# Kernel optimization log

Measured on AMD Instinct MI355X. Metric: run time of the kernel, lower is better.

Reference implementation:

```python
import jax, jax.numpy as jnp
import numpy as np

D_MODEL = 1024
LN_EPS = 1e-5


def setup_inputs() -> dict:
    key = jax.random.key(0)
    k_u, k_b, k_c = jax.random.split(key, 3)
    B, L, D = 8, 4096, D_MODEL
    u = jax.random.normal(k_u, (B, L, D), dtype=jnp.float32)
    # parameters (torch init analogues)
    log_a = jnp.log(jnp.linspace(0.9, 0.99, D, dtype=jnp.float32))
    bound = 1.0 / np.sqrt(D)
    W_b = jax.random.uniform(k_b, (D, D), minval=-bound, maxval=bound, dtype=jnp.float32)
    W_c = jax.random.uniform(k_c, (D, D), minval=-bound, maxval=bound, dtype=jnp.float32)
    gamma = jnp.ones((D,), dtype=jnp.float32)
    beta = jnp.zeros((D,), dtype=jnp.float32)
    return {"u": u, "log_a": log_a, "W_b": W_b, "W_c": W_c, "gamma": gamma, "beta": beta}


def reference(u, log_a, W_b, W_c, gamma, beta):
    # u: [B, L, D]; diagonal LTI SSM: state_t = a * state_{t-1} + (u_t @ W_b^T)
    B, L, D = u.shape
    a = jnp.exp(log_a)  # [D]
    u_b = jnp.einsum('bld,ed->ble', u, W_b)  # batched b-projection over all timesteps

    def step(state, ub_t):
        state = a * state + ub_t
        return state, state

    init = jnp.zeros((B, D), dtype=u.dtype)
    _, states = jax.lax.scan(step, init, jnp.swapaxes(u_b, 0, 1))  # [L, B, D]
    states = jnp.swapaxes(states, 0, 1)  # [B, L, D]

    y = jnp.einsum('bld,ed->ble', states, W_c)  # c-projection batched over time

    # LayerNorm over last dim
    mean = jnp.mean(y, axis=-1, keepdims=True)
    var = jnp.mean(jnp.square(y - mean), axis=-1, keepdims=True)
    return gamma * (y - mean) * jax.lax.rsqrt(var + LN_EPS) + beta
```

## Files before the change

kernel.cpp:

```cpp
#include <hip/hip_runtime.h>
#include <hip/hip_bf16.h>
#include <math.h>

#define B_SZ 8
#define L_SZ 4096
#define D_SZ 1024
#define CHT  64
#define NCH  (L_SZ / CHT)

typedef __bf16 bf16_t;
typedef bf16_t bf16x8 __attribute__((ext_vector_type(8)));
typedef bf16_t bf16x4 __attribute__((ext_vector_type(4)));
typedef float  f32x4  __attribute__((ext_vector_type(4)));

#define BM 256
#define BN 256
#define BK 32
#define NT (1024 / BK)
#define BUFB 32768
#define EP_P 68

__device__ __forceinline__ void gld16(const void* g, void* l) {
  __builtin_amdgcn_global_load_lds(
      (const __attribute__((address_space(1))) void*)g,
      (__attribute__((address_space(3))) void*)l, 16, 0, 0);
}

template<int MODE>
__global__ __launch_bounds__(512, 2)
void gemm256(const bf16_t* __restrict__ A, const bf16_t* __restrict__ Wt,
             bf16_t* __restrict__ Cg, const float* __restrict__ pw,
             float* __restrict__ cf) {
  __shared__ __align__(16) char smem[98304];
  const int tid  = threadIdx.x;
  const int lane = tid & 63;
  const int wave = tid >> 6;
  const int wm = wave >> 2, wn = wave & 3;
  const int fr = lane & 15, g = lane >> 4;

  const int flat = (blockIdx.x & 7) * 64 + (blockIdx.x >> 3);
  const int bx = flat & 3, by = flat >> 2;
  const int brow = by * BM, bcol = bx * BN;

  const int rA = lane >> 2, cA = lane & 3;
  const int sS = (rA ^ (lane >> 4)) & 3;
  const int scol = ((cA ^ sS) << 3);
  const bf16_t* a0 = A  + (size_t)(brow + wave * 16 + rA) * 1024 + scol;
  const bf16_t* a1 = a0 + (size_t)128 * 1024;
  const bf16_t* b0 = Wt + (size_t)(bcol + wave * 16 + rA) * 1024 + scol;
  const bf16_t* b1 = b0 + (size_t)128 * 1024;

  const int sR  = (fr ^ (fr >> 2)) & 3;
  const int rch = ((g ^ sR) << 4);
  const int aoffB = (wm * 128 + fr) * 64 + rch;
  const int boffB = (wn * 64 + fr) * 64 + rch;

  f32x4 acc[8][4] = {};

#define STAGE(BU, T) { \
    char* d_ = smem + (BU) * BUFB + wave * 1024; \
    const int ko_ = (T) * BK; \
    gld16(a0 + ko_, d_); \
    gld16(a1 + ko_, d_ + 8192); \
    gld16(b0 + ko_, d_ + 16384); \
    gld16(b1 + ko_, d_ + 24576); \
  }

  STAGE(0, 0)
  STAGE(1, 1)
  asm volatile("s_waitcnt vmcnt(4)" ::: "memory");
  __builtin_amdgcn_s_barrier();
  asm volatile("" ::: "memory");

  int bu = 0, bs = 2;
  for (int t = 0; t < NT; ++t) {
    const char* aB = smem + bu * BUFB;
    const char* bB = aB + 16384;
    bf16x8 af[8], bfv[4];
#pragma unroll
    for (int mi = 0; mi < 8; ++mi) af[mi] = *(const bf16x8*)(aB + aoffB + mi * 1024);
#pragma unroll
    for (int ni = 0; ni < 4; ++ni) bfv[ni] = *(const bf16x8*)(bB + boffB + ni * 1024);
    if (t + 2 < NT) STAGE(bs, t + 2)
    __builtin_amdgcn_s_setprio(1);
#pragma unroll
    for (int mi = 0; mi < 8; ++mi)
#pragma unroll
      for (int ni = 0; ni < 4; ++ni)
        acc[mi][ni] = __builtin_amdgcn_mfma_f32_16x16x32_bf16(af[mi], bfv[ni], acc[mi][ni], 0, 0, 0);
    __builtin_amdgcn_s_setprio(0);
    if (t + 2 < NT) asm volatile("s_waitcnt vmcnt(4)" ::: "memory");
    else            asm volatile("s_waitcnt vmcnt(0)" ::: "memory");
    __builtin_amdgcn_s_barrier();
    asm volatile("" ::: "memory");
    bu = (bu == 2) ? 0 : bu + 1;
    bs = (bs == 2) ? 0 : bs + 1;
  }
#undef STAGE

  __syncthreads();
  float* strip = (float*)smem;
  const int bb  = by >> 4;
  const int cg0 = (by & 15) * 4;
#pragma unroll 1
  for (int q = 0; q < 4; ++q) {
    if (wn == q) {
#pragma unroll
      for (int mi = 0; mi < 8; ++mi)
#pragma unroll
        for (int ni = 0; ni < 4; ++ni)
#pragma unroll
          for (int r = 0; r < 4; ++r)
            strip[(wm * 128 + mi * 16 + g * 4 + r) * EP_P + ni * 16 + fr] = acc[mi][ni][r];
    }
    __syncthreads();
    if constexpr (MODE == 0) {
      if (tid < 256) {
        const int col = tid & 63;
        const int ch  = tid >> 6;
        const int d   = bcol + q * 64 + col;
        const float a = pw[d];
        float s = 0.f;
#pragma unroll 1
        for (int grp = 0; grp < 4; ++grp) {
          float v[16];
#pragma unroll
          for (int u = 0; u < 16; ++u) v[u] = strip[(ch * 64 + grp * 16 + u) * EP_P + col];
#pragma unroll
          for (int u = 0; u < 16; ++u) { s = a * s + v[u]; v[u] = s; }
#pragma unroll
          for (int u = 0; u < 16; ++u) strip[(ch * 64 + grp * 16 + u) * EP_P + col] = v[u];
        }
        cf[((size_t)(bb * NCH + cg0 + ch)) * D_SZ + d] = s;
      }
      __syncthreads();
    }
#pragma unroll
    for (int j = 0; j < 4; ++j) {
      const int u = j * 512 + tid;
      const int row = u >> 3;
      const int cu = (u & 7) * 8;
      f32x4 lo = *(const f32x4*)&strip[row * EP_P + cu];
      f32x4 hi = *(const f32x4*)&strip[row * EP_P + cu + 4];
      bf16x8 h;
#pragma unroll
      for (int jj = 0; jj < 4; ++jj) { h[jj] = (bf16_t)lo[jj]; h[4 + jj] = (bf16_t)hi[jj]; }
      *(bf16x8*)&Cg[(size_t)(brow + row) * 1024 + bcol + q * 64 + cu] = h;
    }
    __syncthreads();
  }
}

__global__ __launch_bounds__(256)
void conv_bf16_k(const float* __restrict__ src, bf16_t* __restrict__ dst, int n) {
  int i = (blockIdx.x * 256 + threadIdx.x) * 4;
  const int stride = gridDim.x * 256 * 4;
  for (; i < n; i += stride) {
    f32x4 v = *(const f32x4*)(src + i);
    bf16x4 h;
#pragma unroll
    for (int j = 0; j < 4; ++j) h[j] = (bf16_t)v[j];
    *(bf16x4*)(dst + i) = h;
  }
}

__global__ __launch_bounds__(256)
void pow_k(const float* __restrict__ log_a, float* __restrict__ pw) {
  const int t = blockIdx.x;
  const int d = threadIdx.x * 4;
#pragma unroll
  for (int j = 0; j < 4; ++j)
    pw[t * D_SZ + d + j] = expf(log_a[d + j] * (float)(t + 1));
}

__global__ __launch_bounds__(256)
void scan_carry_k(const float* __restrict__ log_a, float* __restrict__ cf) {
  const int d = blockIdx.x * 256 + threadIdx.x;
  const int b = blockIdx.y;
  const float aT = expf(log_a[d] * (float)CHT);
  float s = 0.f;
  for (int c = 0; c < NCH; ++c) {
    const size_t idx = ((size_t)(b * NCH + c)) * D_SZ + d;
    s = aT * s + cf[idx];
    cf[idx] = s;
  }
}

__global__ __launch_bounds__(256)
void scan_apply_k(const bf16_t* __restrict__ xb16, const float* __restrict__ pw,
                  const float* __restrict__ cf, bf16_t* __restrict__ xs16) {
  const int d4 = threadIdx.x * 4;
  const int l = blockIdx.x;
  const int b = blockIdx.y;
  const int c = l >> 6;
  const int t = l & (CHT - 1);
  const size_t idx = ((size_t)(b * L_SZ + l)) * D_SZ + d4;
  bf16x4 hv = *(const bf16x4*)(xb16 + idx);
  f32x4 s;
#pragma unroll
  for (int j = 0; j < 4; ++j) s[j] = (float)hv[j];
  if (c > 0) {
    f32x4 p  = *(const f32x4*)(pw + t * D_SZ + d4);
    f32x4 cv = *(const f32x4*)(cf + ((size_t)(b * NCH + (c - 1))) * D_SZ + d4);
    s += p * cv;
  }
  bf16x4 h;
#pragma unroll
  for (int j = 0; j < 4; ++j) h[j] = (bf16_t)s[j];
  *(bf16x4*)(xs16 + idx) = h;
}

__global__ __launch_bounds__(256)
void ln_k(const bf16_t* __restrict__ y, const float* __restrict__ gamma,
          const float* __restrict__ beta, float* __restrict__ out) {
  const size_t row = blockIdx.x;
  const int tid = threadIdx.x;
  bf16x4 h = *(const bf16x4*)(y + row * D_SZ + tid * 4);
  float v[4];
#pragma unroll
  for (int j = 0; j < 4; ++j) v[j] = (float)h[j];
  float s  = v[0] + v[1] + v[2] + v[3];
  float sq = v[0] * v[0] + v[1] * v[1] + v[2] * v[2] + v[3] * v[3];
#pragma unroll
  for (int off = 32; off; off >>= 1) {
    s  += __shfl_down(s, off);
    sq += __shfl_down(sq, off);
  }
  __shared__ float red[8];
  const int wid = tid >> 6;
  if ((tid & 63) == 0) { red[wid] = s; red[4 + wid] = sq; }
  __syncthreads();
  s  = red[0] + red[1] + red[2] + red[3];
  sq = red[4] + red[5] + red[6] + red[7];
  const float mean = s * (1.f / D_SZ);
  const float var  = sq * (1.f / D_SZ) - mean * mean;
  const float inv  = rsqrtf(var + 1e-5f);
  f32x4 gm = *(const f32x4*)(gamma + tid * 4);
  f32x4 bt = *(const f32x4*)(beta  + tid * 4);
  f32x4 o;
#pragma unroll
  for (int j = 0; j < 4; ++j) o[j] = (v[j] - mean) * inv * gm[j] + bt[j];
  *(f32x4*)(out + row * D_SZ + tid * 4) = o;
}

extern "C" void kernel_launch(void* const* d_in, const int* in_sizes, int n_in,
                              void* d_out, int out_size, void* d_ws, size_t ws_size,
                              hipStream_t stream) {
  const float* u     = (const float*)d_in[0];
  const float* log_a = (const float*)d_in[1];
  const float* W_b   = (const float*)d_in[2];
  const float* W_c   = (const float*)d_in[3];
  const float* gamma = (const float*)d_in[4];
  const float* beta  = (const float*)d_in[5];
  float* out = (float*)d_out;

  const size_t NBLD = (size_t)B_SZ * L_SZ * D_SZ;
  bf16_t* u16  = (bf16_t*)d_ws;
  bf16_t* xb16 = u16 + NBLD;
  bf16_t* wb16 = xb16 + NBLD;
  bf16_t* wc16 = wb16 + (size_t)D_SZ * D_SZ;
  float*  cf   = (float*)(wc16 + (size_t)D_SZ * D_SZ);
  float*  pw   = cf + (size_t)B_SZ * NCH * D_SZ;
  bf16_t* xs16 = u16;
  bf16_t* y16  = xb16;

  const int nblk = (B_SZ * L_SZ / BM) * (D_SZ / BN);

  conv_bf16_k<<<2048, 256, 0, stream>>>(u, u16, (int)NBLD);
  conv_bf16_k<<<512, 256, 0, stream>>>(W_b, wb16, D_SZ * D_SZ);
  conv_bf16_k<<<512, 256, 0, stream>>>(W_c, wc16, D_SZ * D_SZ);
  pow_k<<<CHT, 256, 0, stream>>>(log_a, pw);

  gemm256<0><<<nblk, 512, 0, stream>>>(u16, wb16, xb16, pw, cf);
  scan_carry_k<<<dim3(D_SZ / 256, B_SZ), 256, 0, stream>>>(log_a, cf);
  scan_apply_k<<<dim3(L_SZ, B_SZ), 256, 0, stream>>>(xb16, pw, cf, xs16);
  gemm256<1><<<nblk, 512, 0, stream>>>(xs16, wc16, y16, nullptr, nullptr);
  ln_k<<<B_SZ * L_SZ, 256, 0, stream>>>(y16, gamma, beta, out);
}
```

Before: 268.0 us.

## Retile GEMM to 256x128x64 with 2x4 wave grid and widen scan_apply vectors

Changes the GEMM block tile from 256x256 with K-step 32 to 256x128 with K-step 64. The wave layout becomes 4x2, each wave holds a 64x64 sub-tile, and the LDS swizzle and staging are rebuilt for 128-byte rows across three 48KB buffers. This doubles the grid and halves per-thread accumulators, aiming for better occupancy and fewer loop iterations and barriers. The cost is lower arithmetic intensity per block and more LDS per block, which may limit residency. scan_apply now processes 8 bf16 elements per thread with 128 threads for wider memory accesses.

```diff
diff --git a/kernel.cpp b/kernel.cpp
--- a/kernel.cpp
+++ b/kernel.cpp
@@ -14,10 +14,10 @@
 typedef float  f32x4  __attribute__((ext_vector_type(4)));
 
 #define BM 256
-#define BN 256
-#define BK 32
+#define BN 128
+#define BK 64
 #define NT (1024 / BK)
-#define BUFB 32768
+#define BUFB 49152
 #define EP_P 68
 
 __device__ __forceinline__ void gld16(const void* g, void* l) {
@@ -31,65 +31,72 @@
 void gemm256(const bf16_t* __restrict__ A, const bf16_t* __restrict__ Wt,
              bf16_t* __restrict__ Cg, const float* __restrict__ pw,
              float* __restrict__ cf) {
-  __shared__ __align__(16) char smem[98304];
+  __shared__ __align__(16) char smem[3 * BUFB];
   const int tid  = threadIdx.x;
   const int lane = tid & 63;
   const int wave = tid >> 6;
-  const int wm = wave >> 2, wn = wave & 3;
+  const int wm = wave >> 1, wn = wave & 1;
   const int fr = lane & 15, g = lane >> 4;
 
-  const int flat = (blockIdx.x & 7) * 64 + (blockIdx.x >> 3);
-  const int bx = flat & 3, by = flat >> 2;
+  const int flat = (blockIdx.x & 7) * 128 + (blockIdx.x >> 3);
+  const int bx = flat & 7, by = flat >> 3;
   const int brow = by * BM, bcol = bx * BN;
 
-  const int rA = lane >> 2, cA = lane & 3;
-  const int sS = (rA ^ (lane >> 4)) & 3;
-  const int scol = ((cA ^ sS) << 3);
-  const bf16_t* a0 = A  + (size_t)(brow + wave * 16 + rA) * 1024 + scol;
-  const bf16_t* a1 = a0 + (size_t)128 * 1024;
-  const bf16_t* b0 = Wt + (size_t)(bcol + wave * 16 + rA) * 1024 + scol;
-  const bf16_t* b1 = b0 + (size_t)128 * 1024;
-
-  const int sR  = (fr ^ (fr >> 2)) & 3;
-  const int rch = ((g ^ sR) << 4);
-  const int aoffB = (wm * 128 + fr) * 64 + rch;
-  const int boffB = (wn * 64 + fr) * 64 + rch;
-
-  f32x4 acc[8][4] = {};
+  const int sr = lane >> 3;
+  const int sc = (lane & 7) ^ sr;
+  const bf16_t* a0 = A  + (size_t)(brow + wave * 8 + sr) * 1024 + sc * 8;
+  const bf16_t* b0 = Wt + (size_t)(bcol + wave * 8 + sr) * 1024 + sc * 8;
+
+  const int c0 = ((g)     ^ (fr & 7)) << 4;
+  const int c1 = ((4 + g) ^ (fr & 7)) << 4;
+  const int arowB = (wm * 64 + fr) * 128;
+  const int browB = (wn * 64 + fr) * 128;
+
+  f32x4 acc[4][4] = {};
 
 #define STAGE(BU, T) { \
     char* d_ = smem + (BU) * BUFB + wave * 1024; \
-    const int ko_ = (T) * BK; \
+    const size_t ko_ = (size_t)(T) * BK; \
     gld16(a0 + ko_, d_); \
-    gld16(a1 + ko_, d_ + 8192); \
-    gld16(b0 + ko_, d_ + 16384); \
-    gld16(b1 + ko_, d_ + 24576); \
+    gld16(a0 + (size_t)64 * 1024 + ko_, d_ + 8192); \
+    gld16(a0 + (size_t)128 * 1024 + ko_, d_ + 16384); \
+    gld16(a0 + (size_t)192 * 1024 + ko_, d_ + 24576); \
+    gld16(b0 + ko_, d_ + 32768); \
+    gld16(b0 + (size_t)64 * 1024 + ko_, d_ + 40960); \
   }
 
   STAGE(0, 0)
   STAGE(1, 1)
-  asm volatile("s_waitcnt vmcnt(4)" ::: "memory");
+  asm volatile("s_waitcnt vmcnt(6)" ::: "memory");
   __builtin_amdgcn_s_barrier();
   asm volatile("" ::: "memory");
 
   int bu = 0, bs = 2;
   for (int t = 0; t < NT; ++t) {
     const char* aB = smem + bu * BUFB;
-    const char* bB = aB + 16384;
-    bf16x8 af[8], bfv[4];
-#pragma unroll
-    for (int mi = 0; mi < 8; ++mi) af[mi] = *(const bf16x8*)(aB + aoffB + mi * 1024);
-#pragma unroll
-    for (int ni = 0; ni < 4; ++ni) bfv[ni] = *(const bf16x8*)(bB + boffB + ni * 1024);
+    const char* bB = aB + 32768;
+    bf16x8 af[4][2], bfv[4][2];
+#pragma unroll
+    for (int mi = 0; mi < 4; ++mi) {
+      af[mi][0] = *(const bf16x8*)(aB + arowB + mi * 2048 + c0);
+      af[mi][1] = *(const bf16x8*)(aB + arowB + mi * 2048 + c1);
+    }
+#pragma unroll
+    for (int ni = 0; ni < 4; ++ni) {
+      bfv[ni][0] = *(const bf16x8*)(bB + browB + ni * 2048 + c0);
+      bfv[ni][1] = *(const bf16x8*)(bB + browB + ni * 2048 + c1);
+    }
     if (t + 2 < NT) STAGE(bs, t + 2)
     __builtin_amdgcn_s_setprio(1);
 #pragma unroll
-    for (int mi = 0; mi < 8; ++mi)
-#pragma unroll
-      for (int ni = 0; ni < 4; ++ni)
-        acc[mi][ni] = __builtin_amdgcn_mfma_f32_16x16x32_bf16(af[mi], bfv[ni], acc[mi][ni], 0, 0, 0);
+    for (int mi = 0; mi < 4; ++mi)
+#pragma unroll
+      for (int ni = 0; ni < 4; ++ni) {
+        acc[mi][ni] = __builtin_amdgcn_mfma_f32_16x16x32_bf16(af[mi][0], bfv[ni][0], acc[mi][ni], 0, 0, 0);
+        acc[mi][ni] = __builtin_amdgcn_mfma_f32_16x16x32_bf16(af[mi][1], bfv[ni][1], acc[mi][ni], 0, 0, 0);
+      }
     __builtin_amdgcn_s_setprio(0);
-    if (t + 2 < NT) asm volatile("s_waitcnt vmcnt(4)" ::: "memory");
+    if (t + 2 < NT) asm volatile("s_waitcnt vmcnt(6)" ::: "memory");
     else            asm volatile("s_waitcnt vmcnt(0)" ::: "memory");
     __builtin_amdgcn_s_barrier();
     asm volatile("" ::: "memory");
@@ -103,15 +110,15 @@
   const int bb  = by >> 4;
   const int cg0 = (by & 15) * 4;
 #pragma unroll 1
-  for (int q = 0; q < 4; ++q) {
+  for (int q = 0; q < 2; ++q) {
     if (wn == q) {
 #pragma unroll
-      for (int mi = 0; mi < 8; ++mi)
+      for (int mi = 0; mi < 4; ++mi)
 #pragma unroll
         for (int ni = 0; ni < 4; ++ni)
 #pragma unroll
           for (int r = 0; r < 4; ++r)
-            strip[(wm * 128 + mi * 16 + g * 4 + r) * EP_P + ni * 16 + fr] = acc[mi][ni][r];
+            strip[(wm * 64 + mi * 16 + g * 4 + r) * EP_P + ni * 16 + fr] = acc[mi][ni][r];
     }
     __syncthreads();
     if constexpr (MODE == 0) {
@@ -186,28 +193,32 @@
   }
 }
 
-__global__ __launch_bounds__(256)
+__global__ __launch_bounds__(128)
 void scan_apply_k(const bf16_t* __restrict__ xb16, const float* __restrict__ pw,
                   const float* __restrict__ cf, bf16_t* __restrict__ xs16) {
-  const int d4 = threadIdx.x * 4;
+  const int d8 = threadIdx.x * 8;
   const int l = blockIdx.x;
   const int b = blockIdx.y;
   const int c = l >> 6;
   const int t = l & (CHT - 1);
-  const size_t idx = ((size_t)(b * L_SZ + l)) * D_SZ + d4;
-  bf16x4 hv = *(const bf16x4*)(xb16 + idx);
-  f32x4 s;
-#pragma unroll
-  for (int j = 0; j < 4; ++j) s[j] = (float)hv[j];
+  const size_t idx = ((size_t)(b * L_SZ + l)) * D_SZ + d8;
+  bf16x8 hv = *(const bf16x8*)(xb16 + idx);
+  float s[8];
+#pragma unroll
+  for (int j = 0; j < 8; ++j) s[j] = (float)hv[j];
   if (c > 0) {
-    f32x4 p  = *(const f32x4*)(pw + t * D_SZ + d4);
-    f32x4 cv = *(const f32x4*)(cf + ((size_t)(b * NCH + (c - 1))) * D_SZ + d4);
-    s += p * cv;
-  }
-  bf16x4 h;
-#pragma unroll
-  for (int j = 0; j < 4; ++j) h[j] = (bf16_t)s[j];
-  *(bf16x4*)(xs16 + idx) = h;
+    f32x4 p0  = *(const f32x4*)(pw + t * D_SZ + d8);
+    f32x4 p1  = *(const f32x4*)(pw + t * D_SZ + d8 + 4);
+    const float* cb = cf + ((size_t)(b * NCH + (c - 1))) * D_SZ + d8;
+    f32x4 v0 = *(const f32x4*)cb;
+    f32x4 v1 = *(const f32x4*)(cb + 4);
+#pragma unroll
+    for (int j = 0; j < 4; ++j) { s[j] += p0[j] * v0[j]; s[4 + j] += p1[j] * v1[j]; }
+  }
+  bf16x8 h;
+#pragma unroll
+  for (int j = 0; j < 8; ++j) h[j] = (bf16_t)s[j];
+  *(bf16x8*)(xs16 + idx) = h;
 }
 
 __global__ __launch_bounds__(256)
@@ -273,7 +284,7 @@
 
   gemm256<0><<<nblk, 512, 0, stream>>>(u16, wb16, xb16, pw, cf);
   scan_carry_k<<<dim3(D_SZ / 256, B_SZ), 256, 0, stream>>>(log_a, cf);
-  scan_apply_k<<<dim3(L_SZ, B_SZ), 256, 0, stream>>>(xb16, pw, cf, xs16);
+  scan_apply_k<<<dim3(L_SZ, B_SZ), 128, 0, stream>>>(xb16, pw, cf, xs16);
   gemm256<1><<<nblk, 512, 0, stream>>>(xs16, wc16, y16, nullptr, nullptr);
   ln_k<<<B_SZ * L_SZ, 256, 0, stream>>>(y16, gamma, beta, out);
 }
```

After: 267.2 us. About the same (-0.3%).
